# Kernel optimization log

Measured on AMD Instinct MI355X. Metric: run time of the kernel, lower is better.

## Reference

```python
import jax, jax.numpy as jnp
import numpy as np
from jax import lax

DILATIONS = (1, 2, 4)
K = 3        # kernel_size
HORIZON = 6


def _gcn(x, src, dst, W, b, n):
    # PyG GCNConv with self-loops: D^{-1/2}(A+I)D^{-1/2} X W + b
    xw = x @ W                                                # [N,H]
    e = src.shape[0]
    deg = 1.0 + jax.ops.segment_sum(jnp.ones((e,), x.dtype), dst, num_segments=n)
    dinv = lax.rsqrt(deg)                                     # [N]
    msg = xw[src] * (dinv[src] * dinv[dst])[:, None]          # [E,H]
    agg = jax.ops.segment_sum(msg, dst, num_segments=n)       # [N,H]
    return agg + xw * (dinv * dinv)[:, None] + b


def _cell(x, src, dst, win, gcn_w, gcn_b, conv_w, conv_b, proj_w, proj_b):
    n = x.shape[0]
    hg = jax.nn.relu(_gcn(x, src, dst, gcn_w, gcn_b, n))      # [N,H]
    tcn_in = jnp.concatenate([win[:, 1:], hg[:, None]], axis=1)  # [N,K,H]
    hin = jnp.transpose(tcn_in, (0, 2, 1))                    # [N,H,K]
    outs = []
    for i, d in enumerate(DILATIONS):
        p = (K - 1) * d // 2
        y = lax.conv_general_dilated(hin, conv_w[i], (1,), [(p, p)],
                                     rhs_dilation=(d,),
                                     dimension_numbers=('NCH', 'OIH', 'NCH'))
        outs.append(y[:, :, -1] + conv_b[i])                  # last temporal position, [N,H]
    h_new = jnp.concatenate(outs, axis=1) @ proj_w.T + proj_b  # [N,H]
    new_win = jnp.concatenate([win[:, 1:], h_new[:, None]], axis=1)
    return h_new, new_win


def reference(x_seq, edge_index_seq, edge_attr_seq, mask_seq, id_seq,
              gcn_w, gcn_b, conv_w, conv_b, proj_w, proj_b, head_w, head_b):
    T, N, _ = x_seq.shape
    H = gcn_w.shape[1]
    win0 = jnp.zeros((N, K, H), x_seq.dtype)

    def enc_step(win, inp):
        x_t, ei_t = inp
        _, win = _cell(x_t, ei_t[0], ei_t[1], win,
                       gcn_w, gcn_b, conv_w, conv_b, proj_w, proj_b)
        return win, None

    win, _ = lax.scan(enc_step, win0, (x_seq, edge_index_seq))

    src, dst = edge_index_seq[-1, 0], edge_index_seq[-1, 1]

    def dec_step(carry, _):
        win, inp = carry
        h_new, win = _cell(inp, src, dst, win,
                           gcn_w, gcn_b, conv_w, conv_b, proj_w, proj_b)
        y = h_new @ head_w.T + head_b                          # [N,C]
        return (win, y), y

    _, preds = lax.scan(dec_step, (win, x_seq[-1]), None, length=HORIZON)
    return preds  # [horizon, N, out_channels]


def setup_inputs() -> dict:
    T, N, F, E, H, C = 12, 20000, 16, 320000, 128, 16
    key = jax.random.key(0)
    ks = jax.random.split(key, 12)
    return {
        'x_seq': jax.random.normal(ks[0], (T, N, F), jnp.float32),
        'edge_index_seq': jax.random.randint(ks[1], (T, 2, E), 0, N, jnp.int64),
        'edge_attr_seq': jax.random.normal(ks[2], (T, E, 1), jnp.float32),
        'mask_seq': jnp.ones((T, N), jnp.bool_),
        'id_seq': jnp.tile(jnp.arange(N, dtype=jnp.int32)[None], (T, 1)),
        'gcn_w': jax.random.normal(ks[3], (F, H), jnp.float32) * 0.1,
        'gcn_b': jnp.zeros((H,), jnp.float32),
        'conv_w': jax.random.normal(ks[4], (3, H, H, K), jnp.float32) * 0.05,
        'conv_b': jnp.zeros((3, H), jnp.float32),
        'proj_w': jax.random.normal(ks[5], (H, 3 * H), jnp.float32) * 0.05,
        'proj_b': jnp.zeros((H,), jnp.float32),
        'head_w': jax.random.normal(ks[6], (C, H), jnp.float32) * 0.05,
        'head_b': jnp.zeros((C,), jnp.float32),
    }
```

## Files before the change

### kernel.cpp

```cpp
#include <hip/hip_runtime.h>

#define NN 20000
#define NP 20032
#define EE 320000
#define TT 12
#define HH 128
#define FF 16
#define CC 16
#define HOR 6

#define NB 313
#define WPT 84
#define CHE 3812

#define AGG_GRID 1896

typedef __attribute__((ext_vector_type(8))) short short8;
typedef __attribute__((ext_vector_type(4))) float f32x4;

__device__ __forceinline__ float blo(unsigned int u) {
    union { float f; unsigned int i; } v; v.i = u << 16; return v.f;
}
__device__ __forceinline__ float bhi(unsigned int u) {
    union { float f; unsigned int i; } v; v.i = u & 0xffff0000u; return v.f;
}
__device__ __forceinline__ unsigned short f2b(float f) {
    union { float f; unsigned int i; } v; v.f = f;
    unsigned int x = v.i;
    return (unsigned short)((x + 0x7fffu + ((x >> 16) & 1u)) >> 16);
}
__device__ __forceinline__ unsigned int pck(float lo, float hi) {
    return ((unsigned int)f2b(hi) << 16) | f2b(lo);
}
__device__ __forceinline__ void addrow(float* acc, uint4 r) {
    acc[0] += blo(r.x); acc[1] += bhi(r.x);
    acc[2] += blo(r.y); acc[3] += bhi(r.y);
    acc[4] += blo(r.z); acc[5] += bhi(r.z);
    acc[6] += blo(r.w); acc[7] += bhi(r.w);
}

__global__ void k_zero(int* p, int n) {
    int i = blockIdx.x * 256 + threadIdx.x;
    if (i < n) p[i] = 0;
}

__global__ __launch_bounds__(512) void k_binA(const int* __restrict__ ei,
                                              int* __restrict__ gData,
                                              int* __restrict__ pcnt,
                                              int* __restrict__ pofs) {
    int wg = blockIdx.x;
    int t = wg / WPT, w = wg - t * WPT;
    __shared__ int lcnt[NB];
    __shared__ int sm[512];
    __shared__ __align__(16) int elist[CHE];
    int tid = threadIdx.x;
    for (int i = tid; i < NB; i += 512) lcnt[i] = 0;
    __syncthreads();
    int e0 = w * CHE, e1 = min(EE, e0 + CHE);
    int total = e1 - e0;
    const int* si = ei + (size_t)t * 2 * EE;
    const int* di = si + EE;
    int eA = e0 + tid * 4, eB = eA + 2048;
    bool hA = eA < e1, hB = eB < e1;
    int sA[4], dA[4], pA[4], sB[4], dB[4], pB[4];
    if (hA) {
        int4 s4 = *(const int4*)(si + eA);
        int4 d4 = *(const int4*)(di + eA);
        sA[0] = s4.x; sA[1] = s4.y; sA[2] = s4.z; sA[3] = s4.w;
        dA[0] = d4.x; dA[1] = d4.y; dA[2] = d4.z; dA[3] = d4.w;
    }
    if (hB) {
        int4 s4 = *(const int4*)(si + eB);
        int4 d4 = *(const int4*)(di + eB);
        sB[0] = s4.x; sB[1] = s4.y; sB[2] = s4.z; sB[3] = s4.w;
        dB[0] = d4.x; dB[1] = d4.y; dB[2] = d4.z; dB[3] = d4.w;
    }
    if (hA) {
#pragma unroll
        for (int k = 0; k < 4; k++) pA[k] = atomicAdd(&lcnt[dA[k] >> 6], 1);
    }
    if (hB) {
#pragma unroll
        for (int k = 0; k < 4; k++) pB[k] = atomicAdd(&lcnt[dB[k] >> 6], 1);
    }
    __syncthreads();
    sm[tid] = (tid < NB) ? lcnt[tid] : 0;
    __syncthreads();
    for (int off = 1; off < 512; off <<= 1) {
        int u = (tid >= off) ? sm[tid - off] : 0;
        __syncthreads();
        sm[tid] += u;
        __syncthreads();
    }
    if (tid < NB) {
        int v = lcnt[tid];
        int ex = sm[tid] - v;
        size_t o = (size_t)(t * WPT + w) * NB + tid;
        pcnt[o] = v;
        pofs[o] = ex;
        sm[tid] = ex;
    }
    __syncthreads();
    if (hA) {
#pragma unroll
        for (int k = 0; k < 4; k++) {
            int b = dA[k] >> 6;
            elist[sm[b] + pA[k]] = ((dA[k] & 63) << 16) | sA[k];
        }
    }
    if (hB) {
#pragma unroll
        for (int k = 0; k < 4; k++) {
            int b = dB[k] >> 6;
            elist[sm[b] + pB[k]] = ((dB[k] & 63) << 16) | sB[k];
        }
    }
    __syncthreads();
    int* gOut = gData + (size_t)(t * WPT + w) * CHE;
    for (int i = tid * 4; i < total; i += 2048)
        *(int4*)(gOut + i) = *(const int4*)&elist[i];
}

__global__ __launch_bounds__(512) void k_bscan2(const int* __restrict__ pcnt,
                                                int* __restrict__ bbase,
                                                int* __restrict__ rowptr) {
    int t = blockIdx.x, tid = threadIdx.x;
    __shared__ int sm[512];
    int v = 0;
    if (tid < NB)
        for (int w = 0; w < WPT; w++) v += pcnt[(size_t)(t * WPT + w) * NB + tid];
    sm[tid] = v;
    __syncthreads();
    for (int off = 1; off < 512; off <<= 1) {
        int u = (tid >= off) ? sm[tid - off] : 0;
        __syncthreads();
        sm[tid] += u;
        __syncthreads();
    }
    if (tid < NB) bbase[t * NB + tid] = sm[tid] - v;
    if (tid == 511) rowptr[(size_t)t * (NN + 1) + NN] = sm[511];
}

__global__ __launch_bounds__(256) void k_placeB(const int* __restrict__ gData,
                                                const int* __restrict__ pcnt,
                                                const int* __restrict__ pofs,
                                                const int* __restrict__ bbase,
                                                int* __restrict__ rowptr,
                                                float* __restrict__ dinv,
                                                unsigned short* __restrict__ csr) {
    int t = blockIdx.x / NB, b = blockIdx.x - t * NB;
    int tid = threadIdx.x;
    __shared__ int scnt[WPT], sofs[WPT], cofs[WPT + 1];
    __shared__ int elist[2048];
    __shared__ int cnt64[64], lofs[64], place[64];
    if (tid < WPT) {
        size_t o = (size_t)(t * WPT + tid) * NB + b;
        scnt[tid] = pcnt[o];
        sofs[tid] = pofs[o];
    }
    if (tid < 64) cnt64[tid] = 0;
    __syncthreads();
    if (tid == 0) {
        int s = 0;
        for (int w = 0; w < WPT; w++) { cofs[w] = s; s += scnt[w]; }
        cofs[WPT] = s;
    }
    __syncthreads();
    int total = cofs[WPT];
    int wv = tid >> 6, lane = tid & 63;
    for (int w = wv; w < WPT; w += 4) {
        int c = scnt[w], o = cofs[w];
        const int* sp = gData + (size_t)(t * WPT + w) * CHE + sofs[w];
        for (int i = lane; i < c; i += 64) elist[o + i] = sp[i];
    }
    __syncthreads();
    for (int i = tid; i < total; i += 256) atomicAdd(&cnt64[elist[i] >> 16], 1);
    __syncthreads();
    if (tid == 0) {
        int s = 0;
        for (int j = 0; j < 64; j++) { lofs[j] = s; place[j] = s; s += cnt64[j]; }
    }
    __syncthreads();
    int base = bbase[t * NB + b];
    int n = b * 64 + tid;
    if (tid < 64 && n < NN) {
        rowptr[(size_t)t * (NN + 1) + n] = base + lofs[tid];
        dinv[(size_t)t * NN + n] = rsqrtf(1.0f + (float)cnt64[tid]);
    }
    unsigned short* cbase = csr + (size_t)t * EE + base;
    for (int i = tid; i < total; i += 256) {
        int en = elist[i];
        int r = atomicAdd(&place[en >> 16], 1);
        cbase[r] = (unsigned short)(en & 0xffff);
    }
}

__global__ void k_count(const int* __restrict__ ei, int* __restrict__ cnt) {
    int idx = blockIdx.x * 256 + threadIdx.x;
    if (idx >= TT * EE) return;
    int t = idx / EE, e = idx - t * EE;
    int d = ei[t * 2 * EE + EE + e];
    atomicAdd(&cnt[t * NN + d], 1);
}

__global__ void k_dinvF(const int* __restrict__ cnt, float* __restrict__ dinv) {
    int idx = blockIdx.x * 256 + threadIdx.x;
    if (idx >= TT * NN) return;
    dinv[idx] = 1.0f / sqrtf(1.0f + (float)cnt[idx]);
}

__global__ void k_scan(const int* __restrict__ cnt, int* __restrict__ rowptr, int* __restrict__ wofs) {
    int t = blockIdx.x;
    const int* c = cnt + t * NN;
    int* rp = rowptr + t * (NN + 1);
    int* wo = wofs + t * NN;
    __shared__ int sums[1024];
    int tid = threadIdx.x;
    const int CH2 = 20;
    int base = tid * CH2;
    int loc[CH2];
    int s = 0;
    for (int i = 0; i < CH2; i++) { int ix = base + i; int v = (ix < NN) ? c[ix] : 0; loc[i] = s; s += v; }
    sums[tid] = s;
    __syncthreads();
    for (int off = 1; off < 1024; off <<= 1) {
        int v = (tid >= off) ? sums[tid - off] : 0;
        __syncthreads();
        sums[tid] += v;
        __syncthreads();
    }
    int excl = (tid > 0) ? sums[tid - 1] : 0;
    for (int i = 0; i < CH2; i++) {
        int ix = base + i;
        if (ix < NN) { int e = excl + loc[i]; rp[ix] = e; wo[ix] = e; }
    }
    if (tid == 1023) rp[NN] = sums[1023];
}

__global__ void k_place(const int* __restrict__ ei, int* __restrict__ wofs,
                        unsigned short* __restrict__ csr) {
    int idx = blockIdx.x * 256 + threadIdx.x;
    if (idx >= TT * EE) return;
    int t = idx / EE, e = idx - t * EE;
    int s = ei[t * 2 * EE + e];
    int d = ei[t * 2 * EE + EE + e];
    int pos = atomicAdd(&wofs[t * NN + d], 1);
    csr[t * EE + pos] = (unsigned short)s;
}

__global__ void k_wprepB(const float* __restrict__ cw, const float* __restrict__ pw,
                         const float* __restrict__ cb, const float* __restrict__ pb,
                         unsigned short* __restrict__ Bpk, float* __restrict__ Bf32,
                         float* __restrict__ bias) {
    int idx = blockIdx.x * 256 + threadIdx.x;
    if (blockIdx.x == 192) {
        int h = threadIdx.x;
        if (h < HH) {
            float m = pb[h];
            for (int d = 0; d < 3; d++)
                for (int o = 0; o < HH; o++)
                    m += cb[d * HH + o] * pw[h * 384 + d * HH + o];
            bias[h] = m;
        }
        return;
    }
    if (idx >= 384 * HH) return;
    int kk = idx / HH, h = idx - kk * HH;
    float m = 0.f;
    if (kk < 128) {
        int i = kk;
        for (int o = 0; o < HH; o++)
            m += cw[((1 * HH + o) * HH + i) * 3 + 0] * pw[h * 384 + 128 + o];
    } else if (kk < 256) {
        int i = kk - 128;
        for (int o = 0; o < HH; o++)
            m += cw[((0 * HH + o) * HH + i) * 3 + 0] * pw[h * 384 + o];
    } else {
        int i = kk - 256;
        for (int d = 0; d < 3; d++)
            for (int o = 0; o < HH; o++)
                m += cw[((d * HH + o) * HH + i) * 3 + 1] * pw[h * 384 + d * HH + o];
    }
    Bf32[kk * HH + h] = m;
    int ki = kk >> 5, r = kk & 31, q = r >> 3, j = r & 7, nt = h >> 4, ln = q * 16 + (h & 15);
    Bpk[(size_t)((ki * 8 + nt) * 64 + ln) * 8 + j] = f2b(m);
}

__global__ __launch_bounds__(256) void k_packP(const float* __restrict__ Bf32,
                                               const float* __restrict__ biasT,
                                               unsigned short* __restrict__ Bpk2,
                                               float* __restrict__ biasP) {
    int gidx = blockIdx.x * 256 + threadIdx.x;
    if (gidx < 16 * 16 * 64 * 8) {
        int j = gidx & 7, ln = (gidx >> 3) & 63, nt = (gidx >> 9) & 15, kb = gidx >> 13;
        int q = ln >> 4;
        int kk = (kb & 3) * 32 + q * 8 + j;
        int c = nt * 16 + (ln & 15);
        int s = c >> 7, h = c & 127;
        int g = kb >> 2;
        const float* M2 = Bf32;
        const float* M1 = Bf32 + 128 * HH;
        const float* Mh = Bf32 + 256 * HH;
        float v = 0.f;
        if (g == 0) {
            if (s == 0) v = M2[kk * HH + h];
            else { for (int o = 0; o < HH; o++) v += M2[kk * HH + o] * M1[o * HH + h]; }
        } else if (g == 1) {
            if (s == 0) v = M1[kk * HH + h];
            else {
                v = M2[kk * HH + h];
                for (int o = 0; o < HH; o++) v += M1[kk * HH + o] * M1[o * HH + h];
            }
        } else if (g == 2) {
            if (s == 0) v = Mh[kk * HH + h];
            else { for (int o = 0; o < HH; o++) v += Mh[kk * HH + o] * M1[o * HH + h]; }
        } else {
            v = (s == 0) ? 0.f : Mh[kk * HH + h];
        }
        Bpk2[gidx] = f2b(v);
    } else if (gidx < 16 * 16 * 64 * 8 + 256) {
        int c = gidx - 16 * 16 * 64 * 8;
        if (c < 128) biasP[c] = biasT[c];
        else {
            int h = c & 127;
            float v = biasT[h];
            const float* M1 = Bf32 + 128 * HH;
            for (int o = 0; o < HH; o++) v += biasT[o] * M1[o * HH + h];
            biasP[c] = v;
        }
    }
}

__global__ void k_xs(const float* __restrict__ x, const float* __restrict__ dinv,
                     unsigned short* __restrict__ xs) {
    int idx = blockIdx.x * 256 + threadIdx.x;
    if (idx >= TT * NN) return;
    float dn = dinv[idx];
    const float4* xr = (const float4*)(x + (size_t)idx * FF);
    unsigned int res[8];
#pragma unroll
    for (int k = 0; k < 4; k++) {
        float4 v = xr[k];
        res[2 * k]     = pck(v.x * dn, v.y * dn);
        res[2 * k + 1] = pck(v.z * dn, v.w * dn);
    }
    uint4* dst = (uint4*)(xs + (size_t)idx * FF);
    dst[0] = *(uint4*)(res);
    dst[1] = *(uint4*)(res + 4);
}

__global__ __launch_bounds__(256) void k_aggX(const unsigned short* __restrict__ xsA,
                                              const unsigned short* __restrict__ csrA,
                                              const int* __restrict__ rpA,
                                              const float* __restrict__ dinvA,
                                              float* __restrict__ zA) {
    int bid = blockIdx.x;
    int x = bid & 7, k = bid >> 3;
    int h = 3 * x + k / 79;
    int g = h >> 1;
    int nb = (h & 1) * 79 + (k % 79);
    int tid = threadIdx.x;
    int r = tid >> 1, eo = tid & 1;
    int n = nb * 128 + r;
    if (n >= NN) return;
    const unsigned short* xs = xsA + (size_t)g * NN * FF;
    const unsigned short* csr = csrA + (size_t)g * EE;
    const int* rp = rpA + (size_t)g * (NN + 1);
    float acc[16];
#pragma unroll
    for (int i = 0; i < 16; i++) acc[i] = 0.f;
    int j0 = rp[n], j1 = rp[n + 1];
    int j = j0 + eo;
    for (; j + 2 < j1; j += 4) {
        int s0 = csr[j], s1 = csr[j + 2];
        const uint4* p0 = (const uint4*)(xs + (size_t)s0 * FF);
        const uint4* p1 = (const uint4*)(xs + (size_t)s1 * FF);
        uint4 a0 = p0[0], a1 = p0[1], b0 = p1[0], b1 = p1[1];
        addrow(acc, a0); addrow(acc + 8, a1);
        addrow(acc, b0); addrow(acc + 8, b1);
    }
    if (j < j1) {
        const uint4* p0 = (const uint4*)(xs + (size_t)csr[j] * FF);
        uint4 a0 = p0[0], a1 = p0[1];
        addrow(acc, a0); addrow(acc + 8, a1);
    }
#pragma unroll
    for (int i = 0; i < 16; i++) acc[i] += __shfl_xor(acc[i], 1);
    if (eo == 0) {
        const uint4* sp = (const uint4*)(xs + (size_t)n * FF);
        uint4 a = sp[0], b4 = sp[1];
        addrow(acc, a); addrow(acc + 8, b4);
        float dn = dinvA[(size_t)g * NN + n];
        float4* zo = (float4*)(zA + (size_t)g * NP * FF + (size_t)n * FF);
#pragma unroll
        for (int k2 = 0; k2 < 4; k2++)
            zo[k2] = make_float4(acc[4 * k2] * dn, acc[4 * k2 + 1] * dn,
                                 acc[4 * k2 + 2] * dn, acc[4 * k2 + 3] * dn);
    }
}

__device__ __forceinline__ void hg_frag(const float* zsh, const float* Wg, const float* gbs,
                                        int mr, int q, short8* hgf) {
    float zr[16];
    {
        const float4* zp = (const float4*)(zsh + mr * FF);
        float4 z0 = zp[0], z1 = zp[1], z2 = zp[2], z3 = zp[3];
        zr[0] = z0.x; zr[1] = z0.y; zr[2] = z0.z; zr[3] = z0.w;
        zr[4] = z1.x; zr[5] = z1.y; zr[6] = z1.z; zr[7] = z1.w;
        zr[8] = z2.x; zr[9] = z2.y; zr[10] = z2.z; zr[11] = z2.w;
        zr[12] = z3.x; zr[13] = z3.y; zr[14] = z3.z; zr[15] = z3.w;
    }
#pragma unroll
    for (int k2 = 0; k2 < 4; k2++) {
        float s[8];
#pragma unroll
        for (int c = 0; c < 8; c++) s[c] = gbs[k2 * 32 + q * 8 + c];
#pragma unroll
        for (int f = 0; f < 16; f++) {
            const float4* wp = (const float4*)(Wg + f * HH + k2 * 32 + q * 8);
            float4 w0 = wp[0], w1 = wp[1];
            float zf = zr[f];
            s[0] += zf * w0.x; s[1] += zf * w0.y; s[2] += zf * w0.z; s[3] += zf * w0.w;
            s[4] += zf * w1.x; s[5] += zf * w1.y; s[6] += zf * w1.z; s[7] += zf * w1.w;
        }
#pragma unroll
        for (int c = 0; c < 8; c++) hgf[k2][c] = (short)f2b(fmaxf(s[c], 0.f));
    }
}

__global__ __launch_bounds__(256, 4) void k_gemm2(const unsigned short* __restrict__ a0,
                                                  const unsigned short* __restrict__ a1,
                                                  const float* __restrict__ zA,
                                                  const float* __restrict__ zB,
                                                  const float* __restrict__ gw,
                                                  const float* __restrict__ gb,
                                                  const unsigned short* __restrict__ Bpk2,
                                                  const float* __restrict__ biasP,
                                                  unsigned short* __restrict__ out0,
                                                  unsigned short* __restrict__ out1) {
    __shared__ float Wg[FF * HH];
    __shared__ float zshA[16 * FF], zshB[16 * FF];
    __shared__ float gbs[HH];
    __shared__ float bps[256];
    __shared__ __align__(16) unsigned short hgA[16 * 136], hgB[16 * 136];
    __shared__ __align__(16) unsigned short csh[16 * 264];
    int tid = threadIdx.x;
    int wid = tid >> 6, lane = tid & 63;
    int m0b = blockIdx.x * 16;
    int mr = lane & 15, q = lane >> 4;
    for (int i = tid; i < FF * HH; i += 256) Wg[i] = gw[i];
    if (tid < 16 * FF) {
        zshA[tid] = zA[(size_t)m0b * FF + tid];
        zshB[tid] = zB[(size_t)m0b * FF + tid];
    }
    if (tid < HH) gbs[tid] = gb[tid];
    bps[tid] = biasP[tid];
    __syncthreads();
    if (wid == 0) {
        short8 hgf[4];
        hg_frag(zshA, Wg, gbs, mr, q, hgf);
#pragma unroll
        for (int k2 = 0; k2 < 4; k2++)
            *(short8*)&hgA[mr * 136 + k2 * 32 + q * 8] = hgf[k2];
    } else if (wid == 1) {
        short8 hgf[4];
        hg_frag(zshB, Wg, gbs, mr, q, hgf);
#pragma unroll
        for (int k2 = 0; k2 < 4; k2++)
            *(short8*)&hgB[mr * 136 + k2 * 32 + q * 8] = hgf[k2];
    }
    __syncthreads();
    int nt0 = wid * 4;
    f32x4 acc[4];
#pragma unroll
    for (int j = 0; j < 4; j++) acc[j] = (f32x4){0.f, 0.f, 0.f, 0.f};
#pragma unroll
    for (int kb = 0; kb < 12; kb++) {
        short8 bf[4];
#pragma unroll
        for (int j = 0; j < 4; j++)
            bf[j] = *(const short8*)(Bpk2 + (size_t)((kb * 16 + nt0 + j) * 64 + lane) * 8);
        short8 af;
        if (kb < 4)
            af = *(const short8*)(a0 + (size_t)(m0b + mr) * HH + kb * 32 + q * 8);
        else if (kb < 8)
            af = *(const short8*)(a1 + (size_t)(m0b + mr) * HH + (kb - 4) * 32 + q * 8);
        else
            af = *(const short8*)&hgA[mr * 136 + (kb - 8) * 32 + q * 8];
#pragma unroll
        for (int j = 0; j < 4; j++)
            acc[j] = __builtin_amdgcn_mfma_f32_16x16x32_bf16(af, bf[j], acc[j], 0, 0, 0);
    }
    if (wid >= 2) {
#pragma unroll
        for (int k2 = 0; k2 < 4; k2++) {
            int kb = 12 + k2;
            short8 bf[4];
#pragma unroll
            for (int j = 0; j < 4; j++)
                bf[j] = *(const short8*)(Bpk2 + (size_t)((kb * 16 + nt0 + j) * 64 + lane) * 8);
            short8 af = *(const short8*)&hgB[mr * 136 + k2 * 32 + q * 8];
#pragma unroll
            for (int j = 0; j < 4; j++)
                acc[j] = __builtin_amdgcn_mfma_f32_16x16x32_bf16(af, bf[j], acc[j], 0, 0, 0);
        }
    }
#pragma unroll
    for (int j = 0; j < 4; j++) {
        int c = (nt0 + j) * 16 + mr;
        float bv = bps[c];
#pragma unroll
        for (int r = 0; r < 4; r++)
            csh[(q * 4 + r) * 264 + c] = f2b(acc[j][r] + bv);
    }
    __syncthreads();
#pragma unroll
    for (int i = 0; i < 2; i++) {
        int idx = i * 256 + tid;
        int row = idx >> 5, c8 = (idx & 31) * 8;
        short8 v = *(const short8*)&csh[row * 264 + c8];
        if (c8 < 128) *(short8*)(out0 + (size_t)(m0b + row) * HH + c8) = v;
        else          *(short8*)(out1 + (size_t)(m0b + row) * HH + (c8 - 128)) = v;
    }
}

__global__ __launch_bounds__(256, 3) void k_gemmF2(const unsigned short* __restrict__ a0,
                                                   const unsigned short* __restrict__ a1,
                                                   const float* __restrict__ zt, int gather,
                                                   const float* __restrict__ gw,
                                                   const float* __restrict__ gb,
                                                   const unsigned short* __restrict__ Bpk,
                                                   const float* __restrict__ bias,
                                                   unsigned short* __restrict__ out,
                                                   const float* __restrict__ hw,
                                                   const float* __restrict__ hbv,
                                                   const float* __restrict__ dinvN,
                                                   const int* __restrict__ rp,
                                                   const unsigned short* __restrict__ csr,
                                                   unsigned short* __restrict__ xsD,
                                                   float* __restrict__ yout) {
    __shared__ float Wg[FF * HH];
    __shared__ float Whs[CC * 132];
    __shared__ float gbs[HH], biasS[HH], hbS[CC];
    __shared__ float zsh[16 * FF];
    __shared__ __align__(16) unsigned short hgD[16 * 136];
    __shared__ unsigned short hsh[16 * 136];
    __shared__ float ysh[16 * 17];
    int tid = threadIdx.x;
    int wid = tid >> 6, lane = tid & 63;
    int m0b = blockIdx.x * 16;
    int mr = lane & 15, q = lane >> 4;
    for (int i = tid; i < FF * HH; i += 256) {
        Wg[i] = gw[i];
        Whs[(i >> 7) * 132 + (i & 127)] = hw[i];
    }
    if (tid < HH) { gbs[tid] = gb[tid]; biasS[tid] = bias[tid]; }
    if (tid < CC) hbS[tid] = hbv[tid];
    if (!gather) {
        if (tid < 16 * FF) zsh[tid] = zt[(size_t)m0b * FF + tid];
    } else {
        int r = tid >> 4, p = tid & 15, half = p & 1, eo = p >> 1;
        int n = m0b + r;
        float a[8];
#pragma unroll
        for (int k = 0; k < 8; k++) a[k] = 0.f;
        if (n < NN) {
            int j0 = rp[n], j1 = rp[n + 1];
            for (int j = j0 + eo; j < j1; j += 8) {
                int s = csr[j];
                uint4 v = *(const uint4*)(xsD + (size_t)s * FF + half * 8);
                addrow(a, v);
            }
        }
#pragma unroll
        for (int k = 0; k < 8; k++) {
            a[k] += __shfl_xor(a[k], 2);
            a[k] += __shfl_xor(a[k], 4);
            a[k] += __shfl_xor(a[k], 8);
        }
        if (n < NN && eo == 0) {
            uint4 sv = *(const uint4*)(xsD + (size_t)n * FF + half * 8);
            addrow(a, sv);
            float dn = dinvN[n];
#pragma unroll
            for (int k = 0; k < 8; k++) zsh[r * FF + half * 8 + k] = a[k] * dn;
        }
    }
    __syncthreads();
    if (wid == 0) {
        short8 hgf[4];
        hg_frag(zsh, Wg, gbs, mr, q, hgf);
#pragma unroll
        for (int k2 = 0; k2 < 4; k2++)
            *(short8*)&hgD[mr * 136 + k2 * 32 + q * 8] = hgf[k2];
    }
    __syncthreads();
    int nt0 = wid * 2;
    f32x4 acc[2];
#pragma unroll
    for (int j = 0; j < 2; j++) acc[j] = (f32x4){0.f, 0.f, 0.f, 0.f};
#pragma unroll
    for (int ki = 0; ki < 12; ki++) {
        short8 bf[2];
#pragma unroll
        for (int j = 0; j < 2; j++)
            bf[j] = *(const short8*)(Bpk + (size_t)((ki * 8 + nt0 + j) * 64 + lane) * 8);
        short8 af;
        if (ki < 4)
            af = *(const short8*)(a0 + (size_t)(m0b + mr) * HH + ki * 32 + q * 8);
        else if (ki < 8)
            af = *(const short8*)(a1 + (size_t)(m0b + mr) * HH + (ki - 4) * 32 + q * 8);
        else
            af = *(const short8*)&hgD[mr * 136 + (ki - 8) * 32 + q * 8];
#pragma unroll
        for (int j = 0; j < 2; j++)
            acc[j] = __builtin_amdgcn_mfma_f32_16x16x32_bf16(af, bf[j], acc[j], 0, 0, 0);
    }
#pragma unroll
    for (int j = 0; j < 2; j++) {
        int feat = (nt0 + j) * 16 + mr;
        float bv = biasS[feat];
#pragma unroll
        for (int r = 0; r < 4; r++)
            hsh[(q * 4 + r) * 136 + feat] = f2b(acc[j][r] + bv);
    }
    __syncthreads();
    {
        int row = tid >> 4, c8 = (tid & 15) * 8;
        *(short8*)(out + (size_t)(m0b + row) * HH + c8) =
            *(const short8*)&hsh[row * 136 + c8];
    }
    {
        int r = tid >> 4, c = tid & 15;
        float y = hbS[c];
        for (int k = 0; k < HH; k++)
            y += blo((unsigned int)hsh[r * 136 + k]) * Whs[c * 132 + k];
        ysh[r * 17 + c] = y;
        int gn = m0b + r;
        if (gn < NN) yout[(size_t)gn * CC + c] = y;
    }
    __syncthreads();
    if (tid < 16) {
        int gn = m0b + tid;
        if (gn < NN) {
            float dn = dinvN[gn];
            unsigned int res[8];
#pragma unroll
            for (int k = 0; k < 8; k++)
                res[k] = pck(ysh[tid * 17 + 2 * k] * dn, ysh[tid * 17 + 2 * k + 1] * dn);
            uint4* dst = (uint4*)(xsD + (size_t)gn * FF);
            dst[0] = *(uint4*)(res);
            dst[1] = *(uint4*)(res + 4);
        }
    }
}

extern "C" void kernel_launch(void* const* d_in, const int* in_sizes, int n_in,
                              void* d_out, int out_size, void* d_ws, size_t ws_size,
                              hipStream_t stream) {
    const float* x_seq  = (const float*)d_in[0];
    const int*   ei     = (const int*)d_in[1];
    const float* gcn_w  = (const float*)d_in[5];
    const float* gcn_b  = (const float*)d_in[6];
    const float* conv_w = (const float*)d_in[7];
    const float* conv_b = (const float*)d_in[8];
    const float* proj_w = (const float*)d_in[9];
    const float* proj_b = (const float*)d_in[10];
    const float* head_w = (const float*)d_in[11];
    const float* head_b = (const float*)d_in[12];
    float* outp = (float*)d_out;

    char* ws = (char*)d_ws;
    size_t off = 0;
    auto alloc = [&](size_t bytes) { void* p = ws + off; off += (bytes + 255) & ~(size_t)255; return p; };
    float*          dinv   = (float*)alloc((size_t)TT * NN * 4);
    int*            rowptr = (int*)alloc((size_t)TT * (NN + 1) * 4);
    unsigned short* csr    = (unsigned short*)alloc((size_t)TT * EE * 2);
    unsigned short* hb0    = (unsigned short*)alloc((size_t)NP * HH * 2);
    unsigned short* hb1    = (unsigned short*)alloc((size_t)NP * HH * 2);
    unsigned short* hb2    = (unsigned short*)alloc((size_t)NP * HH * 2);
    unsigned short* hb3    = (unsigned short*)alloc((size_t)NP * HH * 2);
    unsigned short* xsD    = (unsigned short*)alloc((size_t)NP * FF * 2);
    unsigned short* Bpk    = (unsigned short*)alloc((size_t)384 * HH * 2);
    float*          Bf32   = (float*)alloc((size_t)384 * HH * 4);
    float*          biasT  = (float*)alloc(HH * 4);
    unsigned short* Bpk2   = (unsigned short*)alloc((size_t)16 * 16 * 64 * 8 * 2);
    float*          biasP  = (float*)alloc(256 * 4);
    size_t tb = off;
    unsigned short* xs12 = (unsigned short*)alloc((size_t)TT * NN * FF * 2);
    float*          z12  = (float*)alloc((size_t)TT * NP * FF * 4);
    size_t compute_end = off;
    off = tb;
    int* gData = (int*)alloc((size_t)TT * WPT * CHE * 4);
    int* pcnt  = (int*)alloc((size_t)TT * WPT * NB * 4);
    int* pofs  = (int*)alloc((size_t)TT * WPT * NB * 4);
    int* bbase = (int*)alloc((size_t)TT * NB * 4);
    size_t csr_end = off;
    bool fastcsr = (csr_end <= ws_size && compute_end <= ws_size);

    k_zero<<<(NP * HH + 255) / 256, 256, 0, stream>>>((int*)hb2, NP * HH);

    if (fastcsr) {
        k_binA<<<TT * WPT, 512, 0, stream>>>(ei, gData, pcnt, pofs);
        k_bscan2<<<TT, 512, 0, stream>>>(pcnt, bbase, rowptr);
        k_placeB<<<TT * NB, 256, 0, stream>>>(gData, pcnt, pofs, bbase, rowptr, dinv, csr);
    } else {
        off = tb;
        int* cnt  = (int*)alloc((size_t)TT * NN * 4);
        int* wofs = (int*)alloc((size_t)TT * NN * 4);
        k_zero<<<(TT * NN + 255) / 256, 256, 0, stream>>>(cnt, TT * NN);
        k_count<<<(TT * EE + 255) / 256, 256, 0, stream>>>(ei, cnt);
        k_dinvF<<<(TT * NN + 255) / 256, 256, 0, stream>>>(cnt, dinv);
        k_scan<<<TT, 1024, 0, stream>>>(cnt, rowptr, wofs);
        k_place<<<(TT * EE + 255) / 256, 256, 0, stream>>>(ei, wofs, csr);
    }

    k_wprepB<<<193, 256, 0, stream>>>(conv_w, proj_w, conv_b, proj_b, Bpk, Bf32, biasT);
    k_packP<<<(16 * 16 * 64 * 8 + 256 + 255) / 256, 256, 0, stream>>>(Bf32, biasT, Bpk2, biasP);

    k_xs<<<(TT * NN + 255) / 256, 256, 0, stream>>>(x_seq, dinv, xs12);
    k_aggX<<<AGG_GRID, 256, 0, stream>>>(xs12, csr, rowptr, dinv, z12);

    unsigned short* hbuf[4] = {hb0, hb1, hb2, hb3};
    for (int t = 0; t < TT; t += 2) {
        k_gemm2<<<NP / 16, 256, 0, stream>>>(hbuf[(t + 2) & 3], hbuf[(t + 3) & 3],
                                             z12 + (size_t)t * NP * FF,
                                             z12 + (size_t)(t + 1) * NP * FF,
                                             gcn_w, gcn_b, Bpk2, biasP,
                                             hbuf[t & 3], hbuf[(t + 1) & 3]);
    }
    const float* dinv11 = dinv + (size_t)(TT - 1) * NN;
    const int* rp11 = rowptr + (size_t)(TT - 1) * (NN + 1);
    const unsigned short* csr11 = csr + (size_t)(TT - 1) * EE;
    for (int t = TT; t < TT + HOR; t++) {
        const float* zt = (t == TT) ? (z12 + (size_t)(TT - 1) * NP * FF) : nullptr;
        k_gemmF2<<<NP / 16, 256, 0, stream>>>(hbuf[(t + 2) & 3], hbuf[(t + 3) & 3],
                                              zt, (t == TT) ? 0 : 1,
                                              gcn_w, gcn_b, Bpk, biasT, hbuf[t & 3],
                                              head_w, head_b, dinv11, rp11, csr11,
                                              xsD, outp + (size_t)(t - TT) * NN * CC);
    }
}
```

Measured before the change: 468.7 us.

## Unroll linear encoder recurrence into one GEMM over all timestep GCN outputs

The encoder recurrence is linear in the hidden state, so the 12-step chain is unrolled algebraically. A new k_tchain kernel builds the stacked powers of the transition matrices and bias terms, k_hgA computes all GCN activations at once, and a single K=1536 MFMA GEMM (k_gemmE) produces the final two window states. This replaces six sequential k_gemm2 launches and the window zeroing, removing serialization between steps. In exchange it stores a 12-timestep bf16 activation buffer, and the composed weights may accumulate more rounding error.

```diff
diff --git a/kernel.cpp b/kernel.cpp
--- a/kernel.cpp
+++ b/kernel.cpp
@@ -14,6 +14,7 @@
 #define CHE 3812
 
 #define AGG_GRID 1896
+#define HGA_GRID 15024
 
 typedef __attribute__((ext_vector_type(8))) short short8;
 typedef __attribute__((ext_vector_type(4))) float f32x4;
@@ -286,48 +287,63 @@
     Bpk[(size_t)((ki * 8 + nt) * 64 + ln) * 8 + j] = f2b(m);
 }
 
-__global__ __launch_bounds__(256) void k_packP(const float* __restrict__ Bf32,
-                                               const float* __restrict__ biasT,
-                                               unsigned short* __restrict__ Bpk2,
-                                               float* __restrict__ biasP) {
-    int gidx = blockIdx.x * 256 + threadIdx.x;
-    if (gidx < 16 * 16 * 64 * 8) {
-        int j = gidx & 7, ln = (gidx >> 3) & 63, nt = (gidx >> 9) & 15, kb = gidx >> 13;
-        int q = ln >> 4;
-        int kk = (kb & 3) * 32 + q * 8 + j;
-        int c = nt * 16 + (ln & 15);
-        int s = c >> 7, h = c & 127;
-        int g = kb >> 2;
-        const float* M2 = Bf32;
-        const float* M1 = Bf32 + 128 * HH;
-        const float* Mh = Bf32 + 256 * HH;
-        float v = 0.f;
-        if (g == 0) {
-            if (s == 0) v = M2[kk * HH + h];
-            else { for (int o = 0; o < HH; o++) v += M2[kk * HH + o] * M1[o * HH + h]; }
-        } else if (g == 1) {
-            if (s == 0) v = M1[kk * HH + h];
-            else {
-                v = M2[kk * HH + h];
-                for (int o = 0; o < HH; o++) v += M1[kk * HH + o] * M1[o * HH + h];
+__global__ __launch_bounds__(128) void k_tchain(const float* __restrict__ Bf32,
+                                                const float* __restrict__ biasT,
+                                                unsigned short* __restrict__ Bq,
+                                                float* __restrict__ biasQ) {
+    __shared__ float v1[128], v2[128];
+    int c = threadIdx.x;
+    int r = blockIdx.x;
+    const float* M2 = Bf32;
+    const float* M1 = Bf32 + 128 * HH;
+    const float* Mh = Bf32 + 256 * HH;
+    if (r < 128) {
+        int q4 = (r & 31) >> 3, jj = r & 7, rb = r >> 5;
+        v1[c] = Mh[r * HH + c];
+        v2[c] = 0.f;
+        __syncthreads();
+        {
+            float val = v1[c];
+            int kb0 = 10 * 4 + rb, nt0 = c >> 4, ln = q4 * 16 + (c & 15);
+            Bq[((size_t)(kb0 * 16 + nt0) * 64 + ln) * 8 + jj] = f2b(val);
+            int kb1 = 11 * 4 + rb, nt1 = 8 + (c >> 4);
+            Bq[((size_t)(kb1 * 16 + nt1) * 64 + ln) * 8 + jj] = f2b(val);
+        }
+        for (int j = 1; j < 12; j++) {
+            float acc = 0.f;
+            for (int k = 0; k < 128; k++)
+                acc += v1[k] * M1[k * HH + c] + v2[k] * M2[k * HH + c];
+            __syncthreads();
+            v2[c] = v1[c]; v1[c] = acc;
+            __syncthreads();
+            int ln = q4 * 16 + (c & 15);
+            if (j <= 10) {
+                int kb = (10 - j) * 4 + rb, nt = c >> 4;
+                Bq[((size_t)(kb * 16 + nt) * 64 + ln) * 8 + jj] = f2b(acc);
             }
-        } else if (g == 2) {
-            if (s == 0) v = Mh[kk * HH + h];
-            else { for (int o = 0; o < HH; o++) v += Mh[kk * HH + o] * M1[o * HH + h]; }
-        } else {
-            v = (s == 0) ? 0.f : Mh[kk * HH + h];
-        }
-        Bpk2[gidx] = f2b(v);
-    } else if (gidx < 16 * 16 * 64 * 8 + 256) {
-        int c = gidx - 16 * 16 * 64 * 8;
-        if (c < 128) biasP[c] = biasT[c];
-        else {
-            int h = c & 127;
-            float v = biasT[h];
-            const float* M1 = Bf32 + 128 * HH;
-            for (int o = 0; o < HH; o++) v += biasT[o] * M1[o * HH + h];
-            biasP[c] = v;
-        }
+            {
+                int kb = (11 - j) * 4 + rb, nt = 8 + (c >> 4);
+                Bq[((size_t)(kb * 16 + nt) * 64 + ln) * 8 + jj] = f2b(acc);
+            }
+        }
+        {
+            int kb = 11 * 4 + rb, nt = c >> 4, ln = q4 * 16 + (c & 15);
+            Bq[((size_t)(kb * 16 + nt) * 64 + ln) * 8 + jj] = 0;
+        }
+    } else {
+        v1[c] = biasT[c];
+        v2[c] = 0.f;
+        __syncthreads();
+        for (int j = 1; j < 12; j++) {
+            float acc = biasT[c];
+            for (int k = 0; k < 128; k++)
+                acc += v1[k] * M1[k * HH + c] + v2[k] * M2[k * HH + c];
+            __syncthreads();
+            v2[c] = v1[c]; v1[c] = acc;
+            __syncthreads();
+        }
+        biasQ[c] = v2[c];
+        biasQ[128 + c] = v1[c];
     }
 }
 
@@ -399,6 +415,86 @@
     }
 }
 
+__global__ __launch_bounds__(256) void k_hgA(const float* __restrict__ z12,
+                                             const float* __restrict__ gw,
+                                             const float* __restrict__ gb,
+                                             unsigned short* __restrict__ hgAll) {
+    int g = blockIdx.x * 256 + threadIdx.x;
+    int row = g >> 4, cg = g & 15;
+    int c0 = cg * 8;
+    const float4* zp = (const float4*)(z12 + (size_t)row * FF);
+    float4 z0 = zp[0], z1 = zp[1], z2 = zp[2], z3 = zp[3];
+    float zr[16] = {z0.x, z0.y, z0.z, z0.w, z1.x, z1.y, z1.z, z1.w,
+                    z2.x, z2.y, z2.z, z2.w, z3.x, z3.y, z3.z, z3.w};
+    float s[8];
+#pragma unroll
+    for (int c = 0; c < 8; c++) s[c] = gb[c0 + c];
+#pragma unroll
+    for (int f = 0; f < 16; f++) {
+        const float4* wp = (const float4*)(gw + f * HH + c0);
+        float4 w0 = wp[0], w1 = wp[1];
+        float zf = zr[f];
+        s[0] += zf * w0.x; s[1] += zf * w0.y; s[2] += zf * w0.z; s[3] += zf * w0.w;
+        s[4] += zf * w1.x; s[5] += zf * w1.y; s[6] += zf * w1.z; s[7] += zf * w1.w;
+    }
+    unsigned int res[4];
+#pragma unroll
+    for (int k = 0; k < 4; k++)
+        res[k] = pck(fmaxf(s[2 * k], 0.f), fmaxf(s[2 * k + 1], 0.f));
+    *(uint4*)(hgAll + (size_t)row * HH + c0) = *(uint4*)res;
+}
+
+__global__ __launch_bounds__(512, 4) void k_gemmE(const unsigned short* __restrict__ hgAll,
+                                                  const unsigned short* __restrict__ Bq,
+                                                  const float* __restrict__ biasQ,
+                                                  unsigned short* __restrict__ out0,
+                                                  unsigned short* __restrict__ out1) {
+    __shared__ float bqs[256];
+    __shared__ __align__(16) unsigned short csh[32 * 264];
+    int tid = threadIdx.x;
+    int wid = tid >> 6, lane = tid & 63;
+    int rg = wid & 1, cg = wid >> 1;
+    int m0b = blockIdx.x * 32;
+    int m0 = m0b + rg * 16;
+    int mr = lane & 15, q = lane >> 4;
+    if (tid < 256) bqs[tid] = biasQ[tid];
+    int nt0 = cg * 4;
+    f32x4 acc[4];
+#pragma unroll
+    for (int j = 0; j < 4; j++) acc[j] = (f32x4){0.f, 0.f, 0.f, 0.f};
+#pragma unroll
+    for (int kb = 0; kb < 48; kb++) {
+        short8 bf[4];
+#pragma unroll
+        for (int j = 0; j < 4; j++)
+            bf[j] = *(const short8*)(Bq + ((size_t)(kb * 16 + nt0 + j) * 64 + lane) * 8);
+        int s = kb >> 2;
+        short8 af = *(const short8*)(hgAll + ((size_t)(s * NP) + m0 + mr) * HH +
+                                     (kb & 3) * 32 + q * 8);
+#pragma unroll
+        for (int j = 0; j < 4; j++)
+            acc[j] = __builtin_amdgcn_mfma_f32_16x16x32_bf16(af, bf[j], acc[j], 0, 0, 0);
+    }
+    __syncthreads();
+#pragma unroll
+    for (int j = 0; j < 4; j++) {
+        int c = (nt0 + j) * 16 + mr;
+        float bv = bqs[c];
+#pragma unroll
+        for (int r = 0; r < 4; r++)
+            csh[(rg * 16 + q * 4 + r) * 264 + c] = f2b(acc[j][r] + bv);
+    }
+    __syncthreads();
+#pragma unroll
+    for (int i = 0; i < 2; i++) {
+        int idx = i * 512 + tid;
+        int row = idx >> 5, c8 = (idx & 31) * 8;
+        short8 v = *(const short8*)&csh[row * 264 + c8];
+        if (c8 < 128) *(short8*)(out0 + (size_t)(m0b + row) * HH + c8) = v;
+        else          *(short8*)(out1 + (size_t)(m0b + row) * HH + (c8 - 128)) = v;
+    }
+}
+
 __device__ __forceinline__ void hg_frag(const float* zsh, const float* Wg, const float* gbs,
                                         int mr, int q, short8* hgf) {
     float zr[16];
@@ -425,102 +521,6 @@
         }
 #pragma unroll
         for (int c = 0; c < 8; c++) hgf[k2][c] = (short)f2b(fmaxf(s[c], 0.f));
-    }
-}
-
-__global__ __launch_bounds__(256, 4) void k_gemm2(const unsigned short* __restrict__ a0,
-                                                  const unsigned short* __restrict__ a1,
-                                                  const float* __restrict__ zA,
-                                                  const float* __restrict__ zB,
-                                                  const float* __restrict__ gw,
-                                                  const float* __restrict__ gb,
-                                                  const unsigned short* __restrict__ Bpk2,
-                                                  const float* __restrict__ biasP,
-                                                  unsigned short* __restrict__ out0,
-                                                  unsigned short* __restrict__ out1) {
-    __shared__ float Wg[FF * HH];
-    __shared__ float zshA[16 * FF], zshB[16 * FF];
-    __shared__ float gbs[HH];
-    __shared__ float bps[256];
-    __shared__ __align__(16) unsigned short hgA[16 * 136], hgB[16 * 136];
-    __shared__ __align__(16) unsigned short csh[16 * 264];
-    int tid = threadIdx.x;
-    int wid = tid >> 6, lane = tid & 63;
-    int m0b = blockIdx.x * 16;
-    int mr = lane & 15, q = lane >> 4;
-    for (int i = tid; i < FF * HH; i += 256) Wg[i] = gw[i];
-    if (tid < 16 * FF) {
-        zshA[tid] = zA[(size_t)m0b * FF + tid];
-        zshB[tid] = zB[(size_t)m0b * FF + tid];
-    }
-    if (tid < HH) gbs[tid] = gb[tid];
-    bps[tid] = biasP[tid];
-    __syncthreads();
-    if (wid == 0) {
-        short8 hgf[4];
-        hg_frag(zshA, Wg, gbs, mr, q, hgf);
-#pragma unroll
-        for (int k2 = 0; k2 < 4; k2++)
-            *(short8*)&hgA[mr * 136 + k2 * 32 + q * 8] = hgf[k2];
-    } else if (wid == 1) {
-        short8 hgf[4];
-        hg_frag(zshB, Wg, gbs, mr, q, hgf);
-#pragma unroll
-        for (int k2 = 0; k2 < 4; k2++)
-            *(short8*)&hgB[mr * 136 + k2 * 32 + q * 8] = hgf[k2];
-    }
-    __syncthreads();
-    int nt0 = wid * 4;
-    f32x4 acc[4];
-#pragma unroll
-    for (int j = 0; j < 4; j++) acc[j] = (f32x4){0.f, 0.f, 0.f, 0.f};
-#pragma unroll
-    for (int kb = 0; kb < 12; kb++) {
-        short8 bf[4];
-#pragma unroll
-        for (int j = 0; j < 4; j++)
-            bf[j] = *(const short8*)(Bpk2 + (size_t)((kb * 16 + nt0 + j) * 64 + lane) * 8);
-        short8 af;
-        if (kb < 4)
-            af = *(const short8*)(a0 + (size_t)(m0b + mr) * HH + kb * 32 + q * 8);
-        else if (kb < 8)
-            af = *(const short8*)(a1 + (size_t)(m0b + mr) * HH + (kb - 4) * 32 + q * 8);
-        else
-            af = *(const short8*)&hgA[mr * 136 + (kb - 8) * 32 + q * 8];
-#pragma unroll
-        for (int j = 0; j < 4; j++)
-            acc[j] = __builtin_amdgcn_mfma_f32_16x16x32_bf16(af, bf[j], acc[j], 0, 0, 0);
-    }
-    if (wid >= 2) {
-#pragma unroll
-        for (int k2 = 0; k2 < 4; k2++) {
-            int kb = 12 + k2;
-            short8 bf[4];
-#pragma unroll
-            for (int j = 0; j < 4; j++)
-                bf[j] = *(const short8*)(Bpk2 + (size_t)((kb * 16 + nt0 + j) * 64 + lane) * 8);
-            short8 af = *(const short8*)&hgB[mr * 136 + k2 * 32 + q * 8];
-#pragma unroll
-            for (int j = 0; j < 4; j++)
-                acc[j] = __builtin_amdgcn_mfma_f32_16x16x32_bf16(af, bf[j], acc[j], 0, 0, 0);
-        }
-    }
-#pragma unroll
-    for (int j = 0; j < 4; j++) {
-        int c = (nt0 + j) * 16 + mr;
-        float bv = bps[c];
-#pragma unroll
-        for (int r = 0; r < 4; r++)
-            csh[(q * 4 + r) * 264 + c] = f2b(acc[j][r] + bv);
-    }
-    __syncthreads();
-#pragma unroll
-    for (int i = 0; i < 2; i++) {
-        int idx = i * 256 + tid;
-        int row = idx >> 5, c8 = (idx & 31) * 8;
-        short8 v = *(const short8*)&csh[row * 264 + c8];
-        if (c8 < 128) *(short8*)(out0 + (size_t)(m0b + row) * HH + c8) = v;
-        else          *(short8*)(out1 + (size_t)(m0b + row) * HH + (c8 - 128)) = v;
     }
 }
 
@@ -684,11 +684,12 @@
     unsigned short* Bpk    = (unsigned short*)alloc((size_t)384 * HH * 2);
     float*          Bf32   = (float*)alloc((size_t)384 * HH * 4);
     float*          biasT  = (float*)alloc(HH * 4);
-    unsigned short* Bpk2   = (unsigned short*)alloc((size_t)16 * 16 * 64 * 8 * 2);
-    float*          biasP  = (float*)alloc(256 * 4);
     size_t tb = off;
-    unsigned short* xs12 = (unsigned short*)alloc((size_t)TT * NN * FF * 2);
-    float*          z12  = (float*)alloc((size_t)TT * NP * FF * 4);
+    unsigned short* xs12  = (unsigned short*)alloc((size_t)TT * NN * FF * 2);
+    float*          z12   = (float*)alloc((size_t)TT * NP * FF * 4);
+    unsigned short* hgAll = (unsigned short*)alloc((size_t)TT * NP * HH * 2);
+    unsigned short* Bq    = (unsigned short*)alloc((size_t)48 * 16 * 64 * 8 * 2);
+    float*          biasQ = (float*)alloc(256 * 4);
     size_t compute_end = off;
     off = tb;
     int* gData = (int*)alloc((size_t)TT * WPT * CHE * 4);
@@ -697,8 +698,6 @@
     int* bbase = (int*)alloc((size_t)TT * NB * 4);
     size_t csr_end = off;
     bool fastcsr = (csr_end <= ws_size && compute_end <= ws_size);
-
-    k_zero<<<(NP * HH + 255) / 256, 256, 0, stream>>>((int*)hb2, NP * HH);
 
     if (fastcsr) {
         k_binA<<<TT * WPT, 512, 0, stream>>>(ei, gData, pcnt, pofs);
@@ -716,19 +715,14 @@
     }
 
     k_wprepB<<<193, 256, 0, stream>>>(conv_w, proj_w, conv_b, proj_b, Bpk, Bf32, biasT);
-    k_packP<<<(16 * 16 * 64 * 8 + 256 + 255) / 256, 256, 0, stream>>>(Bf32, biasT, Bpk2, biasP);
+    k_tchain<<<129, 128, 0, stream>>>(Bf32, biasT, Bq, biasQ);
 
     k_xs<<<(TT * NN + 255) / 256, 256, 0, stream>>>(x_seq, dinv, xs12);
     k_aggX<<<AGG_GRID, 256, 0, stream>>>(xs12, csr, rowptr, dinv, z12);
+    k_hgA<<<HGA_GRID, 256, 0, stream>>>(z12, gcn_w, gcn_b, hgAll);
+    k_gemmE<<<NP / 32, 512, 0, stream>>>(hgAll, Bq, biasQ, hb2, hb3);
 
     unsigned short* hbuf[4] = {hb0, hb1, hb2, hb3};
-    for (int t = 0; t < TT; t += 2) {
-        k_gemm2<<<NP / 16, 256, 0, stream>>>(hbuf[(t + 2) & 3], hbuf[(t + 3) & 3],
-                                             z12 + (size_t)t * NP * FF,
-                                             z12 + (size_t)(t + 1) * NP * FF,
-                                             gcn_w, gcn_b, Bpk2, biasP,
-                                             hbuf[t & 3], hbuf[(t + 1) & 3]);
-    }
     const float* dinv11 = dinv + (size_t)(TT - 1) * NN;
     const int* rp11 = rowptr + (size_t)(TT - 1) * (NN + 1);
     const unsigned short* csr11 = csr + (size_t)(TT - 1) * EE;
```

New measurement: 498.8 us. 6.4% more time.
